# Optimization experiments

Measured on AMD Instinct MI355X. Metric: run time of the kernel, lower is better.

## Reference

```python
import jax, jax.numpy as jnp
import numpy as np

K = 3
STRIDE = 1
PAD = 1
C_IN = 128
C_OUT = 128
B, H, W = 4, 128, 128


def conv2d(x, w, b, stride, pad):
    # x: (B,C,H,W), w: (O,I,kh,kw)
    out = jax.lax.conv_general_dilated(
        x, w, window_strides=(stride, stride),
        padding=[(pad, pad), (pad, pad)],
        dimension_numbers=("NCHW", "OIHW", "NCHW"))
    return out + b[None, :, None, None]


def bilinear_sample(img, ix, iy):
    # img: (C,H,W); ix, iy: (N,) float pixel coords.
    # Bilinear, padding_mode='zeros', align_corners=False semantics.
    C, Hc, Wc = img.shape
    x0 = jnp.floor(ix).astype(jnp.int32)
    y0 = jnp.floor(iy).astype(jnp.int32)
    x1 = x0 + 1
    y1 = y0 + 1
    wx1 = ix - x0.astype(img.dtype)
    wy1 = iy - y0.astype(img.dtype)
    wx0 = 1.0 - wx1
    wy0 = 1.0 - wy1

    def gather(yi, xi):
        valid = ((yi >= 0) & (yi < Hc) & (xi >= 0) & (xi < Wc)).astype(img.dtype)
        v = img[:, jnp.clip(yi, 0, Hc - 1), jnp.clip(xi, 0, Wc - 1)]  # (C,N)
        return v * valid[None, :]

    return (gather(y0, x0) * (wy0 * wx0)[None]
            + gather(y0, x1) * (wy0 * wx1)[None]
            + gather(y1, x0) * (wy1 * wx0)[None]
            + gather(y1, x1) * (wy1 * wx1)[None])


def setup_inputs() -> dict:
    key = jax.random.key(0)
    k1, k2, k3 = jax.random.split(key, 3)
    x = jax.random.normal(k1, (B, C_IN, H, W), dtype=jnp.float32)
    # offset conv: small random so grid_sample does real irregular gathers
    w_off = jax.random.normal(k2, (2 * K * K, C_IN, K, K), dtype=jnp.float32) * 0.01
    b_off = jnp.zeros((2 * K * K,), dtype=jnp.float32)
    # main conv: kaiming normal, fan_out = C_OUT*K*K
    std = float(np.sqrt(2.0 / (C_OUT * K * K)))
    w_main = jax.random.normal(k3, (C_OUT, C_IN, K, K), dtype=jnp.float32) * std
    b_main = jnp.zeros((C_OUT,), dtype=jnp.float32)
    return {"x": x, "w_off": w_off, "b_off": b_off,
            "w_main": w_main, "b_main": b_main}


def reference(x, w_off, b_off, w_main, b_main):
    Bx, C, Hx, Wx = x.shape
    off = conv2d(x, w_off, b_off, STRIDE, PAD)        # (B, 2*K*K, Ho, Wo)
    Ho, Wo = off.shape[2], off.shape[3]
    off = off.transpose(0, 2, 3, 1).reshape(Bx, Ho, Wo, K, K, 2)
    # snake cumulative offsets: x-offset cumsum over kernel row i, y over col j
    off_x = jnp.cumsum(off[..., 0], axis=3)           # over first kernel dim
    off_y = jnp.cumsum(off[..., 1], axis=4)           # over second kernel dim
    off = jnp.stack([off_x, off_y], axis=-1).reshape(Bx, Ho, Wo, K * K, 2)

    yr = jnp.linspace(-1.0, 1.0, Ho, dtype=x.dtype)
    xr = jnp.linspace(-1.0, 1.0, Wo, dtype=x.dtype)
    yg, xg = jnp.meshgrid(yr, xr, indexing="ij")
    base = jnp.stack([xg, yg], axis=-1)[None, :, :, None, :]  # (1,Ho,Wo,1,2)
    grid = (base + off).reshape(Bx, -1, 2)            # (B, Ho*Wo*K*K, 2)

    # unnormalize (align_corners=False)
    ix = ((grid[..., 0] + 1.0) * Wx - 1.0) * 0.5
    iy = ((grid[..., 1] + 1.0) * Hx - 1.0) * 0.5
    sampled = jax.vmap(bilinear_sample)(x, ix, iy)    # (B, C, Ho*Wo*K*K)
    sampled = sampled.reshape(Bx, C, Ho, Wo, K * K)

    w = w_main.reshape(w_main.shape[0], C, K * K)     # (O, C, K*K)
    out = jnp.einsum("bchwk,ock->bohw", sampled, w)
    return out + b_main[None, :, None, None]
```

## Files before the change

### kernel.cpp

```cpp
#include <hip/hip_runtime.h>
#include <cstddef>

#define Bb   4
#define CI   128
#define CO   128
#define Hh   128
#define Ww   128
#define HW   (Hh*Ww)
#define NOFF 18
#define NTAP 9
#define KTOT (NTAP*CI)
#define NSTEP 36

typedef short short8 __attribute__((ext_vector_type(8)));
typedef _Float16 half8 __attribute__((ext_vector_type(8)));
typedef float floatx4 __attribute__((ext_vector_type(4)));

__device__ inline unsigned short bf16_rne_bits(float f) {
    unsigned u = __float_as_uint(f);
    unsigned r = u + 0x7FFFu + ((u >> 16) & 1u);
    return (unsigned short)(r >> 16);
}
__device__ inline float bf16_bits_to_f32(unsigned short h) {
    return __uint_as_float((unsigned)h << 16);
}
__device__ inline unsigned short f32_to_f16_bits(float f) {
    union { _Float16 h; unsigned short u; } cv;
    cv.h = (_Float16)f;
    return cv.u;
}

__global__ __launch_bounds__(256) void k_transpose(const float* __restrict__ x,
                                                   float* __restrict__ xt,
                                                   _Float16* __restrict__ xt16) {
    __shared__ float tile[32][33];
    int b  = blockIdx.z;
    int c0 = blockIdx.y * 32;
    int p0 = blockIdx.x * 32;
    int tx = threadIdx.x;
    int ty = threadIdx.y;
    const float* xb   = x    + (size_t)b * CI * HW;
    float*       xtb  = xt   + (size_t)b * HW * CI;
    _Float16*    xt16b = xt16 + (size_t)b * HW * CI;
#pragma unroll
    for (int i = 0; i < 4; ++i) {
        int c = c0 + ty + 8 * i;
        tile[ty + 8 * i][tx] = xb[(size_t)c * HW + p0 + tx];
    }
    __syncthreads();
#pragma unroll
    for (int i = 0; i < 4; ++i) {
        int p = p0 + ty + 8 * i;
        float v = tile[tx][ty + 8 * i];
        xtb[(size_t)p * CI + c0 + tx] = v;
        xt16b[(size_t)p * CI + c0 + tx] = (_Float16)v;
    }
}

__global__ __launch_bounds__(256) void k_weights(const float* __restrict__ w_off,
                                                 const float* __restrict__ w_main,
                                                 unsigned short* __restrict__ wofh,
                                                 unsigned short* __restrict__ wofl,
                                                 unsigned short* __restrict__ wf16) {
    int idx = blockIdx.x * 256 + threadIdx.x;
    int stride = gridDim.x * 256;
    for (int i = idx; i < 9 * 4 * 2 * 512; i += stride) {
        int j  = i & 7;
        int l  = (i >> 3) & 63;
        int nt = (i >> 9) & 1;
        int ks = (i >> 10) & 3;
        int t  = i >> 12;
        int oc = nt * 16 + (l & 15);
        int c  = ks * 32 + (l >> 4) * 8 + j;
        float f = (oc < NOFF) ? w_off[(oc * CI + c) * 9 + t] : 0.f;
        unsigned short hb = bf16_rne_bits(f);
        wofh[i] = hb;
        wofl[i] = bf16_rne_bits(f - bf16_bits_to_f32(hb));
    }
    for (int i = idx; i < CO * KTOT; i += stride) {
        int j  = i & 7;
        int l  = (i >> 3) & 63;
        int g  = (i >> 9) & 7;
        int ks = (i >> 12) & 3;
        int t  = i >> 14;
        int o  = g * 16 + (l & 15);
        int c  = ks * 32 + (l >> 4) * 8 + j;
        wf16[i] = f32_to_f16_bits(w_main[(o * CI + c) * 9 + t]);
    }
}

__global__ __launch_bounds__(256, 2) void k_offsets(const float* __restrict__ xt,
                                                    const unsigned short* __restrict__ wofh,
                                                    const unsigned short* __restrict__ wofl,
                                                    const float* __restrict__ b_off,
                                                    float2* __restrict__ coords) {
    __shared__ __align__(16) unsigned short ph[3 * 34 * 128];
    __shared__ __align__(16) unsigned short pl[3 * 34 * 128];
    __shared__ float raw[32][19];
    int blk = blockIdx.x;
    int wt  = blk & 3;
    int h   = (blk >> 2) & 127;
    int b   = blk >> 9;
    int w0  = wt * 32;
    int tid  = threadIdx.x;
    int lane = tid & 63;
    int wave = tid >> 6;

    for (int i = tid; i < 3 * 34 * 64; i += 256) {
        int c2  = i & 63;
        int col = (i >> 6) % 34;
        int r   = i / (34 * 64);
        int gy  = h - 1 + r;
        int gx  = w0 - 1 + col;
        float2 v = make_float2(0.f, 0.f);
        if (gy >= 0 && gy < Hh && gx >= 0 && gx < Ww)
            v = *(const float2*)(xt + (((size_t)b * Hh + gy) * Ww + gx) * CI + c2 * 2);
        unsigned short h0 = bf16_rne_bits(v.x);
        unsigned short h1 = bf16_rne_bits(v.y);
        unsigned l0 = bf16_rne_bits(v.x - bf16_bits_to_f32(h0));
        unsigned l1 = bf16_rne_bits(v.y - bf16_bits_to_f32(h1));
        int byte = (((r * 34 + col) * 128) + c2 * 2) * 2;
        byte ^= (col & 7) << 4;
        *(unsigned*)((char*)ph + byte) = (unsigned)h0 | ((unsigned)h1 << 16);
        *(unsigned*)((char*)pl + byte) = l0 | (l1 << 16);
    }
    __syncthreads();

    int m   = wave & 1;
    int nt  = wave >> 1;
    int l15 = lane & 15, lhi = lane >> 4;
    floatx4 accE = (floatx4){0.f, 0.f, 0.f, 0.f};
    floatx4 accO = (floatx4){0.f, 0.f, 0.f, 0.f};
    const short8* bhp = (const short8*)wofh;
    const short8* blp = (const short8*)wofl;
#pragma unroll
    for (int t = 0; t < 9; ++t) {
        int ki = t / 3, kj = t % 3;
        int colb = m * 16 + l15 + kj;
        int rowoff = (ki * 34 + colb) * 256;
#pragma unroll
        for (int ks = 0; ks < 4; ++ks) {
            int abyte = (rowoff + ks * 64 + lhi * 16) ^ ((colb & 7) << 4);
            short8 Ah = *(const short8*)((char*)ph + abyte);
            short8 Al = *(const short8*)((char*)pl + abyte);
            size_t bi = (size_t)((t * 4 + ks) * 2 + nt) * 64 + lane;
            short8 Bh = bhp[bi];
            short8 Bl = blp[bi];
            floatx4& a = (ks & 1) ? accO : accE;
            a = __builtin_amdgcn_mfma_f32_16x16x32_bf16(Ah, Bh, a, 0, 0, 0);
            a = __builtin_amdgcn_mfma_f32_16x16x32_bf16(Ah, Bl, a, 0, 0, 0);
            a = __builtin_amdgcn_mfma_f32_16x16x32_bf16(Al, Bh, a, 0, 0, 0);
        }
    }
    int oc = nt * 16 + l15;
    if (oc < NOFF) {
        float bo = b_off[oc];
#pragma unroll
        for (int r = 0; r < 4; ++r) {
            int px = m * 16 + lhi * 4 + r;
            raw[px][oc] = (accE[r] + accO[r]) + bo;
        }
    }
    __syncthreads();

    for (int i = tid; i < 32 * NTAP; i += 256) {
        int px = i / NTAP;
        int t  = i % NTAP;
        int ki = t / 3, kj = t % 3;
        float offx = 0.f, offy = 0.f;
        for (int q = 0; q <= ki; ++q) offx += raw[px][q * 6 + kj * 2 + 0];
        for (int q = 0; q <= kj; ++q) offy += raw[px][ki * 6 + q * 2 + 1];
        int wg = w0 + px;
        float xg = -1.0f + 2.0f * (float)wg / 127.0f;
        float yg = -1.0f + 2.0f * (float)h  / 127.0f;
        float gx = xg + offx;
        float gy = yg + offy;
        float ix = ((gx + 1.0f) * (float)Ww - 1.0f) * 0.5f;
        float iy = ((gy + 1.0f) * (float)Hh - 1.0f) * 0.5f;
        coords[(((size_t)b * Hh + h) * Ww + wg) * NTAP + t] = make_float2(ix, iy);
    }
}

__global__ __launch_bounds__(256) void k_sample(const _Float16* __restrict__ xt16,
                                                const float2* __restrict__ coords,
                                                unsigned short* __restrict__ af16,
                                                int q0) {
    int nb = gridDim.x;
    int blkid = blockIdx.x;
    int cpx = nb >> 3;
    blkid = (blkid & 7) * cpx + (blkid >> 3);
    int task = blkid * 4 + (threadIdx.x >> 6);
    int lane = threadIdx.x & 63;
    int Pl   = task / 9;
    int tap  = task - Pl * 9;
    int r = lane & 15, q = lane >> 4;
    int p = q0 + Pl * 16 + r;
    int b = p >> 14;

    float2 co = coords[(size_t)p * NTAP + tap];
    float ix = co.x, iy = co.y;
    float fx0 = floorf(ix), fy0 = floorf(iy);
    int x0 = (int)fx0, y0 = (int)fy0;
    int x1 = x0 + 1,   y1 = y0 + 1;
    float wx1 = ix - fx0, wy1 = iy - fy0;
    float wx0 = 1.f - wx1, wy0 = 1.f - wy1;
    bool vx0 = (x0 >= 0) & (x0 < Ww);
    bool vx1 = (x1 >= 0) & (x1 < Ww);
    bool vy0 = (y0 >= 0) & (y0 < Hh);
    bool vy1 = (y1 >= 0) & (y1 < Hh);
    int cx0 = min(max(x0, 0), Ww - 1), cx1 = min(max(x1, 0), Ww - 1);
    int cy0 = min(max(y0, 0), Hh - 1), cy1 = min(max(y1, 0), Hh - 1);
    float w00 = (vy0 && vx0) ? wy0 * wx0 : 0.f;
    float w01 = (vy0 && vx1) ? wy0 * wx1 : 0.f;
    float w10 = (vy1 && vx0) ? wy1 * wx0 : 0.f;
    float w11 = (vy1 && vx1) ? wy1 * wx1 : 0.f;

    const _Float16* xb  = xt16 + (size_t)b * HW * CI + q * 8;
    const _Float16* r00 = xb + ((size_t)cy0 * Ww + cx0) * CI;
    const _Float16* r01 = xb + ((size_t)cy0 * Ww + cx1) * CI;
    const _Float16* r10 = xb + ((size_t)cy1 * Ww + cx0) * CI;
    const _Float16* r11 = xb + ((size_t)cy1 * Ww + cx1) * CI;
    size_t obase = ((size_t)(Pl * 36 + tap * 4) * 64 + lane) * 8;

#pragma unroll
    for (int ks = 0; ks < 4; ++ks) {
        int c = ks * 32;
        half8 a8 = *(const half8*)(r00 + c);
        half8 b8 = *(const half8*)(r01 + c);
        half8 c8 = *(const half8*)(r10 + c);
        half8 d8 = *(const half8*)(r11 + c);
        short8 hv;
#pragma unroll
        for (int j = 0; j < 8; ++j) {
            float v = w00 * (float)a8[j] + w01 * (float)b8[j]
                    + w10 * (float)c8[j] + w11 * (float)d8[j];
            hv[j] = (short)f32_to_f16_bits(v);
        }
        *(short8*)(af16 + obase + (size_t)ks * 512) = hv;
    }
}

__global__ __launch_bounds__(256, 4) void k_gemm(const unsigned short* __restrict__ af16,
                                                 const unsigned short* __restrict__ wf16,
                                                 const float* __restrict__ b_main,
                                                 float* __restrict__ out, int q0) {
    __shared__ __align__(16) float epi[CO * 33];
    int nb = gridDim.x;
    int cpx = nb >> 3;
    int blk = blockIdx.x;
    blk = (blk & 7) * cpx + (blk >> 3);
    int tid = threadIdx.x, lane = tid & 63, wave = tid >> 6;
    int wave_n = wave & 1, wave_m = wave >> 1;
    int l15 = lane & 15, lhi = lane >> 4;
    int P = blk * 2 + wave_m;

    const half8* ah = (const half8*)af16 + (size_t)P * NSTEP * 64 + lane;
    const half8* bh = (const half8*)wf16 + (size_t)wave_n * 4 * 64 + lane;

    floatx4 acc[4];
#pragma unroll
    for (int n = 0; n < 4; ++n) acc[n] = (floatx4){0.f, 0.f, 0.f, 0.f};

    half8 A0, B0[4], A1, B1[4];
    A0 = ah[0];
#pragma unroll
    for (int n = 0; n < 4; ++n) B0[n] = bh[(size_t)n * 64];

#pragma unroll 2
    for (int s = 0; s < NSTEP; s += 2) {
        A1 = ah[(size_t)(s + 1) * 64];
#pragma unroll
        for (int n = 0; n < 4; ++n) B1[n] = bh[(size_t)((s + 1) * 8 + n) * 64];
#pragma unroll
        for (int n = 0; n < 4; ++n)
            acc[n] = __builtin_amdgcn_mfma_f32_16x16x32_f16(A0, B0[n], acc[n], 0, 0, 0);
        if (s + 2 < NSTEP) {
            A0 = ah[(size_t)(s + 2) * 64];
#pragma unroll
            for (int n = 0; n < 4; ++n) B0[n] = bh[(size_t)((s + 2) * 8 + n) * 64];
        }
#pragma unroll
        for (int n = 0; n < 4; ++n)
            acc[n] = __builtin_amdgcn_mfma_f32_16x16x32_f16(A1, B1[n], acc[n], 0, 0, 0);
    }

#pragma unroll
    for (int n = 0; n < 4; ++n) {
        int o = wave_n * 64 + n * 16 + l15;
#pragma unroll
        for (int rr = 0; rr < 4; ++rr) {
            int px = wave_m * 16 + lhi * 4 + rr;
            epi[o * 33 + px] = acc[n][rr];
        }
    }
    __syncthreads();
    int p_blk = q0 + blk * 32;
    int b = p_blk >> 14, hw = p_blk & 16383;
    float* ob = out + (size_t)b * CO * HW + hw;
    for (int i = tid; i < CO * 32; i += 256) {
        int o  = i >> 5;
        int px = i & 31;
        __builtin_nontemporal_store(epi[o * 33 + px] + b_main[o],
                                    &ob[(size_t)o * HW + px]);
    }
}

extern "C" void kernel_launch(void* const* d_in, const int* in_sizes, int n_in,
                              void* d_out, int out_size, void* d_ws, size_t ws_size,
                              hipStream_t stream) {
    const float* x      = (const float*)d_in[0];
    const float* w_off  = (const float*)d_in[1];
    const float* b_off  = (const float*)d_in[2];
    const float* w_main = (const float*)d_in[3];
    const float* b_main = (const float*)d_in[4];
    float* out = (float*)d_out;

    char* base = (char*)d_ws;
    float*    xt    = (float*)base;
    _Float16* xt16  = (_Float16*)(base + 33554432);
    float2*   coords = (float2*)(base + 33554432 + 16777216);
    unsigned short* wofh = (unsigned short*)(base + 33554432 + 16777216 + 4718592);
    unsigned short* wofl = wofh + 9 * 4 * 2 * 512;
    unsigned short* wf16 = wofl + 9 * 4 * 2 * 512;
    size_t fixed_b = 33554432 + 16777216 + 4718592
                   + 2 * (9 * 4 * 2 * 512) * 2 + (size_t)CO * KTOT * 2;
    unsigned short* af16 = (unsigned short*)(base + fixed_b);

    size_t avail = (ws_size > fixed_b) ? (ws_size - fixed_b) : 0;
    long long maxpx = (long long)(avail / 2304);
    int chunk = (int)((maxpx / 2048) * 2048);
    if (chunk > 32768) chunk = 32768;
    if (chunk < 2048) chunk = 2048;

    k_transpose<<<dim3(HW / 32, CI / 32, Bb), dim3(32, 8), 0, stream>>>(x, xt, xt16);
    k_weights<<<576, 256, 0, stream>>>(w_off, w_main, wofh, wofl, wf16);
    k_offsets<<<Bb * Hh * (Ww / 32), 256, 0, stream>>>(xt, wofh, wofl, b_off, coords);
    for (int q0 = 0; q0 < Bb * HW; q0 += chunk) {
        int np = Bb * HW - q0; if (np > chunk) np = chunk;
        k_sample<<<(np / 16) * 9 / 4, 256, 0, stream>>>(xt16, coords, af16, q0);
        k_gemm<<<np / 32, 256, 0, stream>>>(af16, wf16, b_main, out, q0);
    }
}
```

Measured before the change: 216.9 us.

## Precompute bf16 hi/lo split in transpose and load offset-conv operands from global

The transpose kernel now writes bf16 high and low halves of x directly, alongside fp16, instead of an fp32 transposed copy. The offset-conv kernel drops its LDS staging of a 3x34 halo tile and reads MFMA A operands straight from global or L2, masking out-of-bounds taps. Its occupancy hint rises to 4 blocks per SM. This removes the fp32 intermediate write and read, the per-block bf16 split, the LDS traffic and a barrier. The cost is redundant global reads of overlapping halo rows across waves and tiles.

```diff
diff --git a/kernel.cpp b/kernel.cpp
--- a/kernel.cpp
+++ b/kernel.cpp
@@ -31,17 +31,17 @@
 }
 
 __global__ __launch_bounds__(256) void k_transpose(const float* __restrict__ x,
-                                                   float* __restrict__ xt,
-                                                   _Float16* __restrict__ xt16) {
+                                                   _Float16* __restrict__ xt16,
+                                                   unsigned short* __restrict__ xbh,
+                                                   unsigned short* __restrict__ xbl) {
     __shared__ float tile[32][33];
     int b  = blockIdx.z;
     int c0 = blockIdx.y * 32;
     int p0 = blockIdx.x * 32;
     int tx = threadIdx.x;
     int ty = threadIdx.y;
-    const float* xb   = x    + (size_t)b * CI * HW;
-    float*       xtb  = xt   + (size_t)b * HW * CI;
-    _Float16*    xt16b = xt16 + (size_t)b * HW * CI;
+    const float* xb = x + (size_t)b * CI * HW;
+    size_t obase = (size_t)b * HW * CI;
 #pragma unroll
     for (int i = 0; i < 4; ++i) {
         int c = c0 + ty + 8 * i;
@@ -52,8 +52,11 @@
     for (int i = 0; i < 4; ++i) {
         int p = p0 + ty + 8 * i;
         float v = tile[tx][ty + 8 * i];
-        xtb[(size_t)p * CI + c0 + tx] = v;
-        xt16b[(size_t)p * CI + c0 + tx] = (_Float16)v;
+        size_t o = obase + (size_t)p * CI + c0 + tx;
+        xt16[o] = (_Float16)v;
+        unsigned short hb = bf16_rne_bits(v);
+        xbh[o] = hb;
+        xbl[o] = bf16_rne_bits(v - bf16_bits_to_f32(hb));
     }
 }
 
@@ -89,13 +92,12 @@
     }
 }
 
-__global__ __launch_bounds__(256, 2) void k_offsets(const float* __restrict__ xt,
+__global__ __launch_bounds__(256, 4) void k_offsets(const unsigned short* __restrict__ xbh,
+                                                    const unsigned short* __restrict__ xbl,
                                                     const unsigned short* __restrict__ wofh,
                                                     const unsigned short* __restrict__ wofl,
                                                     const float* __restrict__ b_off,
                                                     float2* __restrict__ coords) {
-    __shared__ __align__(16) unsigned short ph[3 * 34 * 128];
-    __shared__ __align__(16) unsigned short pl[3 * 34 * 128];
     __shared__ float raw[32][19];
     int blk = blockIdx.x;
     int wt  = blk & 3;
@@ -105,51 +107,45 @@
     int tid  = threadIdx.x;
     int lane = tid & 63;
     int wave = tid >> 6;
-
-    for (int i = tid; i < 3 * 34 * 64; i += 256) {
-        int c2  = i & 63;
-        int col = (i >> 6) % 34;
-        int r   = i / (34 * 64);
-        int gy  = h - 1 + r;
-        int gx  = w0 - 1 + col;
-        float2 v = make_float2(0.f, 0.f);
-        if (gy >= 0 && gy < Hh && gx >= 0 && gx < Ww)
-            v = *(const float2*)(xt + (((size_t)b * Hh + gy) * Ww + gx) * CI + c2 * 2);
-        unsigned short h0 = bf16_rne_bits(v.x);
-        unsigned short h1 = bf16_rne_bits(v.y);
-        unsigned l0 = bf16_rne_bits(v.x - bf16_bits_to_f32(h0));
-        unsigned l1 = bf16_rne_bits(v.y - bf16_bits_to_f32(h1));
-        int byte = (((r * 34 + col) * 128) + c2 * 2) * 2;
-        byte ^= (col & 7) << 4;
-        *(unsigned*)((char*)ph + byte) = (unsigned)h0 | ((unsigned)h1 << 16);
-        *(unsigned*)((char*)pl + byte) = l0 | (l1 << 16);
-    }
-    __syncthreads();
-
     int m   = wave & 1;
     int nt  = wave >> 1;
     int l15 = lane & 15, lhi = lane >> 4;
+
     floatx4 accE = (floatx4){0.f, 0.f, 0.f, 0.f};
     floatx4 accO = (floatx4){0.f, 0.f, 0.f, 0.f};
     const short8* bhp = (const short8*)wofh;
     const short8* blp = (const short8*)wofl;
-#pragma unroll
-    for (int t = 0; t < 9; ++t) {
-        int ki = t / 3, kj = t % 3;
-        int colb = m * 16 + l15 + kj;
-        int rowoff = (ki * 34 + colb) * 256;
-#pragma unroll
-        for (int ks = 0; ks < 4; ++ks) {
-            int abyte = (rowoff + ks * 64 + lhi * 16) ^ ((colb & 7) << 4);
-            short8 Ah = *(const short8*)((char*)ph + abyte);
-            short8 Al = *(const short8*)((char*)pl + abyte);
-            size_t bi = (size_t)((t * 4 + ks) * 2 + nt) * 64 + lane;
-            short8 Bh = bhp[bi];
-            short8 Bl = blp[bi];
-            floatx4& a = (ks & 1) ? accO : accE;
-            a = __builtin_amdgcn_mfma_f32_16x16x32_bf16(Ah, Bh, a, 0, 0, 0);
-            a = __builtin_amdgcn_mfma_f32_16x16x32_bf16(Ah, Bl, a, 0, 0, 0);
-            a = __builtin_amdgcn_mfma_f32_16x16x32_bf16(Al, Bh, a, 0, 0, 0);
+    const short8 zero = {0, 0, 0, 0, 0, 0, 0, 0};
+    size_t xbase = (size_t)b * HW * CI + (size_t)lhi * 8;
+    int gx = w0 + m * 16 + l15;
+
+#pragma unroll
+    for (int ki = 0; ki < 3; ++ki) {
+        int gy = h - 1 + ki;
+        bool vy = (gy >= 0) & (gy < Hh);
+        int cy = min(max(gy, 0), Hh - 1);
+#pragma unroll
+        for (int kj = 0; kj < 3; ++kj) {
+            int t = ki * 3 + kj;
+            int gc = gx + kj - 1;
+            bool v = vy & (gc >= 0) & (gc < Ww);
+            int cx = min(max(gc, 0), Ww - 1);
+            size_t rowo = xbase + ((size_t)cy * Ww + cx) * CI;
+            const unsigned short* ph = xbh + rowo;
+            const unsigned short* pl = xbl + rowo;
+#pragma unroll
+            for (int ks = 0; ks < 4; ++ks) {
+                short8 Ah = *(const short8*)(ph + ks * 32);
+                short8 Al = *(const short8*)(pl + ks * 32);
+                if (!v) { Ah = zero; Al = zero; }
+                size_t bi = (size_t)((t * 4 + ks) * 2 + nt) * 64 + lane;
+                short8 Bh = bhp[bi];
+                short8 Bl = blp[bi];
+                floatx4& a = (ks & 1) ? accO : accE;
+                a = __builtin_amdgcn_mfma_f32_16x16x32_bf16(Ah, Bh, a, 0, 0, 0);
+                a = __builtin_amdgcn_mfma_f32_16x16x32_bf16(Ah, Bl, a, 0, 0, 0);
+                a = __builtin_amdgcn_mfma_f32_16x16x32_bf16(Al, Bh, a, 0, 0, 0);
+            }
         }
     }
     int oc = nt * 16 + l15;
@@ -173,10 +169,10 @@
         int wg = w0 + px;
         float xg = -1.0f + 2.0f * (float)wg / 127.0f;
         float yg = -1.0f + 2.0f * (float)h  / 127.0f;
-        float gx = xg + offx;
-        float gy = yg + offy;
-        float ix = ((gx + 1.0f) * (float)Ww - 1.0f) * 0.5f;
-        float iy = ((gy + 1.0f) * (float)Hh - 1.0f) * 0.5f;
+        float gxn = xg + offx;
+        float gyn = yg + offy;
+        float ix = ((gxn + 1.0f) * (float)Ww - 1.0f) * 0.5f;
+        float iy = ((gyn + 1.0f) * (float)Hh - 1.0f) * 0.5f;
         coords[(((size_t)b * Hh + h) * Ww + wg) * NTAP + t] = make_float2(ix, iy);
     }
 }
@@ -316,13 +312,14 @@
     float* out = (float*)d_out;
 
     char* base = (char*)d_ws;
-    float*    xt    = (float*)base;
-    _Float16* xt16  = (_Float16*)(base + 33554432);
-    float2*   coords = (float2*)(base + 33554432 + 16777216);
-    unsigned short* wofh = (unsigned short*)(base + 33554432 + 16777216 + 4718592);
+    _Float16*       xt16 = (_Float16*)base;
+    unsigned short* xbh  = (unsigned short*)(base + 16777216);
+    unsigned short* xbl  = (unsigned short*)(base + 2 * 16777216);
+    float2*         coords = (float2*)(base + 3 * 16777216);
+    unsigned short* wofh = (unsigned short*)(base + 3 * 16777216 + 4718592);
     unsigned short* wofl = wofh + 9 * 4 * 2 * 512;
     unsigned short* wf16 = wofl + 9 * 4 * 2 * 512;
-    size_t fixed_b = 33554432 + 16777216 + 4718592
+    size_t fixed_b = 3ull * 16777216 + 4718592
                    + 2 * (9 * 4 * 2 * 512) * 2 + (size_t)CO * KTOT * 2;
     unsigned short* af16 = (unsigned short*)(base + fixed_b);
 
@@ -332,9 +329,9 @@
     if (chunk > 32768) chunk = 32768;
     if (chunk < 2048) chunk = 2048;
 
-    k_transpose<<<dim3(HW / 32, CI / 32, Bb), dim3(32, 8), 0, stream>>>(x, xt, xt16);
+    k_transpose<<<dim3(HW / 32, CI / 32, Bb), dim3(32, 8), 0, stream>>>(x, xt16, xbh, xbl);
     k_weights<<<576, 256, 0, stream>>>(w_off, w_main, wofh, wofl, wf16);
-    k_offsets<<<Bb * Hh * (Ww / 32), 256, 0, stream>>>(xt, wofh, wofl, b_off, coords);
+    k_offsets<<<Bb * Hh * (Ww / 32), 256, 0, stream>>>(xbh, xbl, wofh, wofl, b_off, coords);
     for (int q0 = 0; q0 < Bb * HW; q0 += chunk) {
         int np = Bb * HW - q0; if (np > chunk) np = chunk;
         k_sample<<<(np / 16) * 9 / 4, 256, 0, stream>>>(xt16, coords, af16, q0);
```

Measured after the change: 236.1 us. 8.8% more time.
